# Optimization experiments

Hardware: AMD Instinct MI355X
Metric: run time of the kernel (lower is better)

The kernel has to match this reference:

```python
import jax, jax.numpy as jnp
import numpy as np

EMB_DIM = 1024
N_HEAD = 16
HEAD_DIM = EMB_DIM // N_HEAD  # 64
NUM_KV = 1
SEQ = 2048
BATCH = 2
QKV_OUT = (N_HEAD + 2 * NUM_KV) * HEAD_DIM  # 1152
ROPE_THETA = 10000.0


def _rope_tables(seq_len, dim):
    inv_freq = 1.0 / (ROPE_THETA ** (jnp.arange(0, dim, 2, dtype=jnp.float32) / dim))  # [dim/2]
    pos = jnp.arange(seq_len, dtype=jnp.float32)
    ang = pos[:, None] * inv_freq[None, :]  # [S, dim/2]
    return jnp.cos(ang), jnp.sin(ang)


def _apply_rope(x, cos, sin):
    # x: [B, S, H, D]; interleaved-pair rotation (torchtune-style)
    B, S, H, D = x.shape
    xr = x.reshape(B, S, H, D // 2, 2)
    x1, x2 = xr[..., 0], xr[..., 1]
    c = cos[None, :, None, :]
    s = sin[None, :, None, :]
    o1 = x1 * c - x2 * s
    o2 = x1 * s + x2 * c
    return jnp.stack([o1, o2], axis=-1).reshape(B, S, H, D)


def setup_inputs() -> dict:
    key = jax.random.key(0)
    k1, k2, k3, k4, k5 = jax.random.split(key, 5)
    scale = 1.0 / np.sqrt(EMB_DIM)
    return {
        "x": jax.random.normal(k1, (BATCH, SEQ, EMB_DIM), dtype=jnp.float32),
        "qkv_w": jax.random.uniform(k2, (QKV_OUT, EMB_DIM), jnp.float32, -scale, scale),
        "qkv_b": jax.random.uniform(k3, (QKV_OUT,), jnp.float32, -scale, scale),
        "out_w": jax.random.uniform(k4, (EMB_DIM, EMB_DIM), jnp.float32, -scale, scale),
        "out_b": jax.random.uniform(k5, (EMB_DIM,), jnp.float32, -scale, scale),
    }


def reference(x, qkv_w, qkv_b, out_w, out_b):
    B, S, E = x.shape
    qkv = x @ qkv_w.T + qkv_b  # [B, S, 1152]
    q_size = N_HEAD * HEAD_DIM
    kv_size = NUM_KV * HEAD_DIM
    q = qkv[..., :q_size].reshape(B, S, N_HEAD, HEAD_DIM)
    k = qkv[..., q_size:q_size + kv_size].reshape(B, S, NUM_KV, HEAD_DIM)
    v = qkv[..., q_size + kv_size:].reshape(B, S, NUM_KV, HEAD_DIM)

    cos, sin = _rope_tables(S, HEAD_DIM)
    q = _apply_rope(q, cos, sin)
    k = _apply_rope(k, cos, sin)

    q = q.transpose(0, 2, 1, 3)  # [B, H, S, D]
    k = k.transpose(0, 2, 1, 3)  # [B, 1, S, D]
    v = v.transpose(0, 2, 1, 3)  # [B, 1, S, D]

    # MQA: single KV head broadcasts over N_HEAD query heads
    scores = jnp.matmul(q, jnp.swapaxes(k, -2, -1)) / np.sqrt(HEAD_DIM)  # [B,H,S,S]
    causal = jnp.tril(jnp.ones((S, S), dtype=bool))
    scores = jnp.where(causal[None, None, :, :], scores, -jnp.inf)
    attn = jax.nn.softmax(scores, axis=-1)
    out = jnp.matmul(attn, v)  # [B, H, S, D]
    out = out.transpose(0, 2, 1, 3).reshape(B, S, E)
    return out @ out_w.T + out_b
```

## Files before the change

kernel.cpp:

```cpp
#include <hip/hip_runtime.h>
#include <stdint.h>
#include <stddef.h>

#define SEQ   2048
#define EMB   1024
#define NHEAD 16
#define HDIM  64
#define QKVO  1152
#define MTOT  4096

typedef __attribute__((ext_vector_type(4))) float f32x4;
typedef __attribute__((ext_vector_type(8))) short short8;
typedef __attribute__((ext_vector_type(4))) short s16x4;

__device__ __forceinline__ short f2bf(float f) {
  union { float f; unsigned u; } v; v.f = f;
  unsigned r = v.u + 0x7FFFu + ((v.u >> 16) & 1u);
  return (short)(r >> 16);
}

__device__ __forceinline__ void gload16(const void* g, void* l) {
  __builtin_amdgcn_global_load_lds((const __attribute__((address_space(1))) void*)g,
                                   (__attribute__((address_space(3))) void*)l,
                                   16, 0, 0);
}

#define PX   524288
#define PW1  671744
#define PW2  802816
#define PTOT 811008

__device__ __forceinline__ void cvt8(const float* __restrict__ s, short* __restrict__ d) {
  float4 a = ((const float4*)s)[0];
  float4 b = ((const float4*)s)[1];
  short8 r;
  r[0]=f2bf(a.x); r[1]=f2bf(a.y); r[2]=f2bf(a.z); r[3]=f2bf(a.w);
  r[4]=f2bf(b.x); r[5]=f2bf(b.y); r[6]=f2bf(b.z); r[7]=f2bf(b.w);
  *(short8*)d = r;
}

__global__ __launch_bounds__(256) void prep_kernel(
    const float* __restrict__ x, const float* __restrict__ wqkv, const float* __restrict__ wout,
    short* __restrict__ xb, short* __restrict__ wqkvb, short* __restrict__ woutb,
    float* __restrict__ cost, float* __restrict__ sint) {
  int c = blockIdx.x * 256 + threadIdx.x;
  if (c < PX) {
    cvt8(x + (size_t)c * 8, xb + (size_t)c * 8);
  } else if (c < PW1) {
    int c2 = c - PX;
    cvt8(wqkv + (size_t)c2 * 8, wqkvb + (size_t)c2 * 8);
  } else if (c < PW2) {
    int c2 = c - PW1;
    cvt8(wout + (size_t)c2 * 8, woutb + (size_t)c2 * 8);
  } else if (c < PTOT) {
    int c2 = c - PW2;
    #pragma unroll
    for (int t = 0; t < 8; ++t) {
      int idx = c2 * 8 + t;
      int pos = idx >> 5, i = idx & 31;
      float inv = powf(10000.0f, -(float)i * (1.0f / 32.0f));
      float ang = (float)pos * inv;
      float sv, cv;
      sincosf(ang, &sv, &cv);
      cost[idx] = cv; sint[idx] = sv;
    }
  }
}

__device__ __forceinline__ void gemm_mainloop(
    const short* __restrict__ A, const short* __restrict__ Bm,
    int m0, int n0, short* lsA, short* lsB, f32x4 acc[4][4]) {
  const int w = threadIdx.x >> 6, lane = threadIdx.x & 63;
  const int wm = w >> 1, wn = w & 1;
  const int lrow = lane & 15, lk = (lane >> 4) * 8;
  #pragma unroll
  for (int mi = 0; mi < 4; ++mi)
    #pragma unroll
    for (int ni = 0; ni < 4; ++ni)
      acc[mi][ni] = (f32x4){0.f, 0.f, 0.f, 0.f};

  const int srow8 = lane >> 3;
  const int scol = (lane & 7) * 8;

  for (int kt = 0; kt < 1024; kt += 64) {
    #pragma unroll
    for (int ii = 0; ii < 4; ++ii) {
      int seg = w * 4 + ii;
      int row = seg * 8 + srow8;
      gload16(A  + (size_t)(m0 + row) * 1024 + kt + scol, lsA + seg * 512);
      gload16(Bm + (size_t)(n0 + row) * 1024 + kt + scol, lsB + seg * 512);
    }
    __syncthreads();
    #pragma unroll
    for (int ks = 0; ks < 2; ++ks) {
      short8 af[4], bfv[4];
      #pragma unroll
      for (int mi = 0; mi < 4; ++mi)
        af[mi] = *(const short8*)(lsA + (wm * 64 + mi * 16 + lrow) * 64 + lk + ks * 32);
      #pragma unroll
      for (int ni = 0; ni < 4; ++ni)
        bfv[ni] = *(const short8*)(lsB + (wn * 64 + ni * 16 + lrow) * 64 + lk + ks * 32);
      #pragma unroll
      for (int mi = 0; mi < 4; ++mi)
        #pragma unroll
        for (int ni = 0; ni < 4; ++ni)
          acc[mi][ni] = __builtin_amdgcn_mfma_f32_16x16x32_bf16(af[mi], bfv[ni], acc[mi][ni], 0, 0, 0);
    }
    __syncthreads();
  }
}

#define QSCALE 0.180336880111124f

__global__ __launch_bounds__(256) void qkv_kernel(
    const short* __restrict__ xb, const short* __restrict__ wb,
    const float* __restrict__ bias, const float* __restrict__ cost, const float* __restrict__ sint,
    short* __restrict__ qbuf, short* __restrict__ kbuf, short* __restrict__ vt) {
  __shared__ __align__(16) short lsA[8192];
  __shared__ __align__(16) short lsB[8192];
  f32x4 acc[4][4];
  const int m0 = blockIdx.x * 128, n0 = blockIdx.y * 128;
  gemm_mainloop(xb, wb, m0, n0, lsA, lsB, acc);

  const int w = threadIdx.x >> 6, lane = threadIdx.x & 63;
  const int wm = w >> 1, wn = w & 1;
  const int colb = n0 + wn * 64 + (lane & 15);
  const int rowb = m0 + wm * 64 + ((lane >> 4) << 2);
  #pragma unroll
  for (int ni = 0; ni < 4; ++ni) {
    const int col = colb + ni * 16;
    const float bv = bias[col];
    #pragma unroll
    for (int mi = 0; mi < 4; ++mi) {
      #pragma unroll
      for (int j = 0; j < 4; ++j) {
        const int m = rowb + mi * 16 + j;
        const int bb = m >> 11, pos = m & 2047;
        float v = acc[mi][ni][j] + bv;
        float vp = __shfl_xor(v, 1);
        float ov;
        if (col < 1088) {
          const int d = (col < 1024) ? (col & 63) : (col - 1024);
          const int i = d >> 1;
          const float cv = cost[pos * 32 + i], sv = sint[pos * 32 + i];
          ov = ((col & 1) == 0) ? (v * cv - vp * sv)
                                : (vp * sv + v * cv);
          if (col < 1024) ov *= QSCALE;
        } else {
          ov = v;
        }
        const short bfo = f2bf(ov);
        if (col < 1024) {
          const int h = col >> 6;
          qbuf[(((size_t)bb * NHEAD + h) * SEQ + pos) * HDIM + (col & 63)] = bfo;
        } else if (col < 1088) {
          kbuf[((size_t)bb * SEQ + pos) * HDIM + (col - 1024)] = bfo;
        } else {
          vt[((size_t)bb * HDIM + (col - 1088)) * SEQ + pos] = bfo;
        }
      }
    }
  }
}

#define PSTRIDE 72

__device__ __forceinline__ void stage_kv(
    const short* __restrict__ kb_b, const short* __restrict__ vt_b, int kv0,
    short* Kb, short* Vb, int tid) {
  #pragma unroll
  for (int rd = 0; rd < 2; ++rd) {
    const int ci = rd * 256 + tid;
    const int r = ci >> 3;
    const int cs = ((ci & 7) * 8) ^ ((r & 7) << 3);
    gload16(kb_b + (size_t)(kv0 + r) * HDIM + cs, Kb + ci * 8);
  }
  #pragma unroll
  for (int rd = 0; rd < 2; ++rd) {
    const int ci = rd * 256 + tid;
    const int r = ci >> 3;
    const int cs = ((ci & 7) * 8) ^ ((r & 7) << 3);
    gload16(vt_b + (size_t)r * SEQ + kv0 + cs, Vb + ci * 8);
  }
}

template<bool MASKED>
__device__ __forceinline__ void attn_tile(
    const short* __restrict__ Kb, const short* __restrict__ Vb,
    int kv0, int qg, int g, int sadr0, int sadr1,
    short* pls,
    short8 qf0, short8 qf1, float& m_run, float& l_run, f32x4 o[4]) {
  f32x4 st[4];
  #pragma unroll
  for (int r = 0; r < 4; ++r) {
    short8 k0 = *(const short8*)(Kb + sadr0 + r * 1024);
    short8 k1 = *(const short8*)(Kb + sadr1 + r * 1024);
    f32x4 z = (f32x4){0.f, 0.f, 0.f, 0.f};
    z = __builtin_amdgcn_mfma_f32_16x16x32_bf16(k0, qf0, z, 0, 0, 0);
    z = __builtin_amdgcn_mfma_f32_16x16x32_bf16(k1, qf1, z, 0, 0, 0);
    st[r] = z;
  }
  float s[16];
  #pragma unroll
  for (int r = 0; r < 4; ++r)
    #pragma unroll
    for (int j = 0; j < 4; ++j) {
      if (MASKED) {
        const int kv = kv0 + r * 16 + g * 4 + j;
        s[r * 4 + j] = (kv <= qg) ? st[r][j] : -1.0e38f;
      } else {
        s[r * 4 + j] = st[r][j];
      }
    }
  float mt = s[0];
  #pragma unroll
  for (int i = 1; i < 16; ++i) mt = fmaxf(mt, s[i]);
  mt = fmaxf(mt, __shfl_xor(mt, 16));
  mt = fmaxf(mt, __shfl_xor(mt, 32));
  if (!__all(mt <= m_run + 11.0f)) {
    const float m_new = fmaxf(m_run, mt);
    const float sc = __builtin_amdgcn_exp2f(m_run - m_new);
    #pragma unroll
    for (int nf = 0; nf < 4; ++nf) o[nf] *= sc;
    l_run *= sc;
    m_run = m_new;
  }
  float p[16], ps = 0.f;
  #pragma unroll
  for (int i = 0; i < 16; ++i) { p[i] = __builtin_amdgcn_exp2f(s[i] - m_run); ps += p[i]; }
  ps += __shfl_xor(ps, 16);
  ps += __shfl_xor(ps, 32);
  l_run += ps;
  #pragma unroll
  for (int r = 0; r < 4; ++r)
    #pragma unroll
    for (int jj = 0; jj < 4; jj += 2) {
      unsigned pk = (unsigned)(unsigned short)f2bf(p[r * 4 + jj]) |
                    ((unsigned)(unsigned short)f2bf(p[r * 4 + jj + 1]) << 16);
      *(unsigned*)(pls + r * 16 + g * 4 + jj) = pk;
    }
  short8 pb0 = *(const short8*)(pls + g * 8);
  short8 pb1 = *(const short8*)(pls + 32 + g * 8);
  #pragma unroll
  for (int nf = 0; nf < 4; ++nf) {
    short8 v0 = *(const short8*)(Vb + sadr0 + nf * 1024);
    short8 v1 = *(const short8*)(Vb + sadr1 + nf * 1024);
    o[nf] = __builtin_amdgcn_mfma_f32_16x16x32_bf16(v0, pb0, o[nf], 0, 0, 0);
    o[nf] = __builtin_amdgcn_mfma_f32_16x16x32_bf16(v1, pb1, o[nf], 0, 0, 0);
  }
}

__global__ __launch_bounds__(256, 3) void attn_kernel(
    const short* __restrict__ qb, const short* __restrict__ kb,
    const short* __restrict__ vt, short* __restrict__ ao) {
  __shared__ __align__(16) short Kls[2][4096];
  __shared__ __align__(16) short Vls[2][4096];
  __shared__ __align__(16) short plds[4][16][PSTRIDE];
  const int tid = threadIdx.x, w = tid >> 6, lane = tid & 63;
  const int bh = blockIdx.x, bb = bh >> 4, h = bh & 15;
  const int qchunk = 31 - blockIdx.y;
  const int q0 = qchunk * 64 + w * 16;
  const int g = lane >> 4, qloc = lane & 15;
  const int qg = q0 + qloc;

  const short* kb_b = kb + (size_t)bb * SEQ * HDIM;
  const short* vt_b = vt + (size_t)bb * HDIM * SEQ;

  const short* qbase = qb + (((size_t)bb * NHEAD + h) * SEQ + q0 + qloc) * HDIM + g * 8;
  short8 qf0 = *(const short8*)qbase;
  short8 qf1 = *(const short8*)(qbase + 32);

  f32x4 o[4];
  #pragma unroll
  for (int nf = 0; nf < 4; ++nf) o[nf] = (f32x4){0.f, 0.f, 0.f, 0.f};
  float m_run = -1.0e38f, l_run = 0.0f;

  short* pls = &plds[w][qloc][0];
  const int swm = (qloc & 7) << 3;
  const int sadr0 = qloc * 64 + ((g * 8) ^ swm);
  const int sadr1 = qloc * 64 + ((g * 8 + 32) ^ swm);

  stage_kv(kb_b, vt_b, 0, Kls[0], Vls[0], tid);
  const int nt = qchunk + 1;
  for (int t = 0; t < nt; ++t) {
    if (t + 1 < nt) {
      stage_kv(kb_b, vt_b, (t + 1) * 64, Kls[(t + 1) & 1], Vls[(t + 1) & 1], tid);
      asm volatile("s_waitcnt vmcnt(4)" ::: "memory");
    } else {
      asm volatile("s_waitcnt vmcnt(0)" ::: "memory");
    }
    __builtin_amdgcn_sched_barrier(0);
    __builtin_amdgcn_s_barrier();
    __builtin_amdgcn_sched_barrier(0);
    const short* Kb = Kls[t & 1];
    const short* Vb = Vls[t & 1];
    if (t + 1 < nt)
      attn_tile<false>(Kb, Vb, t * 64, qg, g, sadr0, sadr1, pls, qf0, qf1, m_run, l_run, o);
    else
      attn_tile<true>(Kb, Vb, t * 64, qg, g, sadr0, sadr1, pls, qf0, qf1, m_run, l_run, o);
    __builtin_amdgcn_sched_barrier(0);
    __builtin_amdgcn_s_barrier();
  }

  const float inv = 1.0f / l_run;
  const size_t obase = ((size_t)bb * SEQ + q0 + qloc) * EMB + (size_t)h * HDIM + g * 4;
  #pragma unroll
  for (int nf = 0; nf < 4; ++nf) {
    s16x4 pk;
    #pragma unroll
    for (int j = 0; j < 4; ++j) pk[j] = f2bf(o[nf][j] * inv);
    *(s16x4*)(ao + obase + nf * 16) = pk;
  }
}

__global__ __launch_bounds__(256) void out_kernel(
    const short* __restrict__ ab, const short* __restrict__ wb,
    const float* __restrict__ bias, float* __restrict__ out) {
  __shared__ __align__(16) short lsA[8192];
  __shared__ __align__(16) short lsB[8192];
  f32x4 acc[4][4];
  const int m0 = blockIdx.x * 128, n0 = blockIdx.y * 128;
  gemm_mainloop(ab, wb, m0, n0, lsA, lsB, acc);

  const int w = threadIdx.x >> 6, lane = threadIdx.x & 63;
  const int wm = w >> 1, wn = w & 1;
  const int colb = n0 + wn * 64 + (lane & 15);
  const int rowb = m0 + wm * 64 + ((lane >> 4) << 2);
  #pragma unroll
  for (int ni = 0; ni < 4; ++ni) {
    const int col = colb + ni * 16;
    const float bv = bias[col];
    #pragma unroll
    for (int mi = 0; mi < 4; ++mi)
      #pragma unroll
      for (int j = 0; j < 4; ++j) {
        const int m = rowb + mi * 16 + j;
        out[(size_t)m * EMB + col] = acc[mi][ni][j] + bv;
      }
  }
}

extern "C" void kernel_launch(void* const* d_in, const int* in_sizes, int n_in,
                              void* d_out, int out_size, void* d_ws, size_t ws_size,
                              hipStream_t stream) {
  const float* x    = (const float*)d_in[0];
  const float* qkvw = (const float*)d_in[1];
  const float* qkvb = (const float*)d_in[2];
  const float* outw = (const float*)d_in[3];
  const float* outb = (const float*)d_in[4];
  float* out = (float*)d_out;
  char* ws = (char*)d_ws;

  short* xb    = (short*)(ws + 0);
  short* wqkvb = (short*)(ws + 8388608);
  short* woutb = (short*)(ws + 10747904);
  float* cost  = (float*)(ws + 12845056);
  float* sint  = (float*)(ws + 13107200);
  short* qbuf  = (short*)(ws + 13369344);
  short* kbuf  = (short*)(ws + 21757952);
  short* vtb   = (short*)(ws + 22282240);
  short* aob   = xb;

  prep_kernel<<<3168, 256, 0, stream>>>(x, qkvw, outw, xb, wqkvb, woutb, cost, sint);
  qkv_kernel<<<dim3(32, 9), 256, 0, stream>>>(xb, wqkvb, qkvb, cost, sint, qbuf, kbuf, vtb);
  attn_kernel<<<dim3(32, 32), 256, 0, stream>>>(qbuf, kbuf, vtb, aob);
  out_kernel<<<dim3(32, 8), 256, 0, stream>>>(aob, woutb, outb, out);
}
```

Before: 192.1 us.

## Double-buffer GEMM mainloop with swizzled LDS and tune attention scheduling

The shared GEMM mainloop now double-buffers its LDS tiles, prefetching the next K tile with global_load_lds while computing the current one, and applies an XOR swizzle to cut LDS bank conflicts. Its launch bounds are set to two blocks per CU because LDS use doubles. The attention kernel gains s_setprio around its MFMA sections, a tree max reduction, a packed bf16 conversion instruction, and a swizzled unpadded P buffer. It also raises occupancy to four blocks and reorders query chunks to balance causal work across the grid. The cost is higher LDS pressure in the GEMMs and relies on the v_cvt_pk_bf16_f32 instruction being available.

Measured after the change: 172.0 us. -10.5%, faster.

```diff
diff --git a/kernel.cpp b/kernel.cpp
--- a/kernel.cpp
+++ b/kernel.cpp
@@ -17,6 +17,12 @@
   union { float f; unsigned u; } v; v.f = f;
   unsigned r = v.u + 0x7FFFu + ((v.u >> 16) & 1u);
   return (short)(r >> 16);
+}
+
+__device__ __forceinline__ unsigned cvtpk_bf16(float lo, float hi) {
+  unsigned r;
+  asm("v_cvt_pk_bf16_f32 %0, %1, %2" : "=v"(r) : "v"(lo), "v"(hi));
+  return r;
 }
 
 __device__ __forceinline__ void gload16(const void* g, void* l) {
@@ -69,7 +75,7 @@
 
 __device__ __forceinline__ void gemm_mainloop(
     const short* __restrict__ A, const short* __restrict__ Bm,
-    int m0, int n0, short* lsA, short* lsB, f32x4 acc[4][4]) {
+    int m0, int n0, short* ls, f32x4 acc[4][4]) {
   const int w = threadIdx.x >> 6, lane = threadIdx.x & 63;
   const int wm = w >> 1, wn = w & 1;
   const int lrow = lane & 15, lk = (lane >> 4) * 8;
@@ -80,47 +86,62 @@
       acc[mi][ni] = (f32x4){0.f, 0.f, 0.f, 0.f};
 
   const int srow8 = lane >> 3;
-  const int scol = (lane & 7) * 8;
-
-  for (int kt = 0; kt < 1024; kt += 64) {
-    #pragma unroll
-    for (int ii = 0; ii < 4; ++ii) {
-      int seg = w * 4 + ii;
-      int row = seg * 8 + srow8;
-      gload16(A  + (size_t)(m0 + row) * 1024 + kt + scol, lsA + seg * 512);
-      gload16(Bm + (size_t)(n0 + row) * 1024 + kt + scol, lsB + seg * 512);
-    }
-    __syncthreads();
+  const int scol = ((lane & 7) * 8) ^ (srow8 << 3);
+  const int rswz = (lrow & 7) << 3;
+
+  #define GSTAGE(buf, kt)                                                     \
+    _Pragma("unroll")                                                         \
+    for (int ii = 0; ii < 4; ++ii) {                                          \
+      int seg = w * 4 + ii;                                                   \
+      int row = seg * 8 + srow8;                                              \
+      gload16(A  + (size_t)(m0 + row) * 1024 + (kt) + scol, (buf) + seg * 512);\
+      gload16(Bm + (size_t)(n0 + row) * 1024 + (kt) + scol, (buf) + 8192 + seg * 512);\
+    }
+
+  GSTAGE(ls, 0);
+  for (int t = 0; t < 16; ++t) {
+    short* cur = ls + (t & 1) * 16384;
+    short* nxt = ls + ((t + 1) & 1) * 16384;
+    if (t < 15) {
+      GSTAGE(nxt, (t + 1) * 64);
+      asm volatile("s_waitcnt vmcnt(8)" ::: "memory");
+    } else {
+      asm volatile("s_waitcnt vmcnt(0)" ::: "memory");
+    }
+    __builtin_amdgcn_sched_barrier(0);
+    __builtin_amdgcn_s_barrier();
+    __builtin_amdgcn_sched_barrier(0);
     #pragma unroll
     for (int ks = 0; ks < 2; ++ks) {
       short8 af[4], bfv[4];
       #pragma unroll
       for (int mi = 0; mi < 4; ++mi)
-        af[mi] = *(const short8*)(lsA + (wm * 64 + mi * 16 + lrow) * 64 + lk + ks * 32);
+        af[mi] = *(const short8*)(cur + (wm * 64 + mi * 16 + lrow) * 64 + ((lk + ks * 32) ^ rswz));
       #pragma unroll
       for (int ni = 0; ni < 4; ++ni)
-        bfv[ni] = *(const short8*)(lsB + (wn * 64 + ni * 16 + lrow) * 64 + lk + ks * 32);
+        bfv[ni] = *(const short8*)(cur + 8192 + (wn * 64 + ni * 16 + lrow) * 64 + ((lk + ks * 32) ^ rswz));
       #pragma unroll
       for (int mi = 0; mi < 4; ++mi)
         #pragma unroll
         for (int ni = 0; ni < 4; ++ni)
           acc[mi][ni] = __builtin_amdgcn_mfma_f32_16x16x32_bf16(af[mi], bfv[ni], acc[mi][ni], 0, 0, 0);
     }
-    __syncthreads();
-  }
+    __builtin_amdgcn_sched_barrier(0);
+    __builtin_amdgcn_s_barrier();
+  }
+  #undef GSTAGE
 }
 
 #define QSCALE 0.180336880111124f
 
-__global__ __launch_bounds__(256) void qkv_kernel(
+__global__ __launch_bounds__(256, 2) void qkv_kernel(
     const short* __restrict__ xb, const short* __restrict__ wb,
     const float* __restrict__ bias, const float* __restrict__ cost, const float* __restrict__ sint,
     short* __restrict__ qbuf, short* __restrict__ kbuf, short* __restrict__ vt) {
-  __shared__ __align__(16) short lsA[8192];
-  __shared__ __align__(16) short lsB[8192];
+  __shared__ __align__(16) short ls[32768];
   f32x4 acc[4][4];
   const int m0 = blockIdx.x * 128, n0 = blockIdx.y * 128;
-  gemm_mainloop(xb, wb, m0, n0, lsA, lsB, acc);
+  gemm_mainloop(xb, wb, m0, n0, ls, acc);
 
   const int w = threadIdx.x >> 6, lane = threadIdx.x & 63;
   const int wm = w >> 1, wn = w & 1;
@@ -163,34 +184,14 @@
   }
 }
 
-#define PSTRIDE 72
-
-__device__ __forceinline__ void stage_kv(
-    const short* __restrict__ kb_b, const short* __restrict__ vt_b, int kv0,
-    short* Kb, short* Vb, int tid) {
-  #pragma unroll
-  for (int rd = 0; rd < 2; ++rd) {
-    const int ci = rd * 256 + tid;
-    const int r = ci >> 3;
-    const int cs = ((ci & 7) * 8) ^ ((r & 7) << 3);
-    gload16(kb_b + (size_t)(kv0 + r) * HDIM + cs, Kb + ci * 8);
-  }
-  #pragma unroll
-  for (int rd = 0; rd < 2; ++rd) {
-    const int ci = rd * 256 + tid;
-    const int r = ci >> 3;
-    const int cs = ((ci & 7) * 8) ^ ((r & 7) << 3);
-    gload16(vt_b + (size_t)r * SEQ + kv0 + cs, Vb + ci * 8);
-  }
-}
-
 template<bool MASKED>
 __device__ __forceinline__ void attn_tile(
     const short* __restrict__ Kb, const short* __restrict__ Vb,
-    int kv0, int qg, int g, int sadr0, int sadr1,
+    int kv0, int qg, int g, int sadr0, int sadr1, int pswz,
     short* pls,
     short8 qf0, short8 qf1, float& m_run, float& l_run, f32x4 o[4]) {
   f32x4 st[4];
+  __builtin_amdgcn_s_setprio(1);
   #pragma unroll
   for (int r = 0; r < 4; ++r) {
     short8 k0 = *(const short8*)(Kb + sadr0 + r * 1024);
@@ -200,6 +201,7 @@
     z = __builtin_amdgcn_mfma_f32_16x16x32_bf16(k1, qf1, z, 0, 0, 0);
     st[r] = z;
   }
+  __builtin_amdgcn_s_setprio(0);
   float s[16];
   #pragma unroll
   for (int r = 0; r < 4; ++r)
@@ -212,9 +214,14 @@
         s[r * 4 + j] = st[r][j];
       }
     }
-  float mt = s[0];
-  #pragma unroll
-  for (int i = 1; i < 16; ++i) mt = fmaxf(mt, s[i]);
+  float a0 = fmaxf(fmaxf(s[0], s[1]), s[2]);
+  float a1 = fmaxf(fmaxf(s[3], s[4]), s[5]);
+  float a2 = fmaxf(fmaxf(s[6], s[7]), s[8]);
+  float a3 = fmaxf(fmaxf(s[9], s[10]), s[11]);
+  float a4 = fmaxf(fmaxf(s[12], s[13]), s[14]);
+  float b0 = fmaxf(fmaxf(a0, a1), a2);
+  float b1 = fmaxf(fmaxf(a3, a4), s[15]);
+  float mt = fmaxf(b0, b1);
   mt = fmaxf(mt, __shfl_xor(mt, 16));
   mt = fmaxf(mt, __shfl_xor(mt, 32));
   if (!__all(mt <= m_run + 11.0f)) {
@@ -235,12 +242,12 @@
   for (int r = 0; r < 4; ++r)
     #pragma unroll
     for (int jj = 0; jj < 4; jj += 2) {
-      unsigned pk = (unsigned)(unsigned short)f2bf(p[r * 4 + jj]) |
-                    ((unsigned)(unsigned short)f2bf(p[r * 4 + jj + 1]) << 16);
-      *(unsigned*)(pls + r * 16 + g * 4 + jj) = pk;
-    }
-  short8 pb0 = *(const short8*)(pls + g * 8);
-  short8 pb1 = *(const short8*)(pls + 32 + g * 8);
+      unsigned pk = cvtpk_bf16(p[r * 4 + jj], p[r * 4 + jj + 1]);
+      *(unsigned*)(pls + ((r * 16 + g * 4 + jj) ^ pswz)) = pk;
+    }
+  short8 pb0 = *(const short8*)(pls + ((g * 8) ^ pswz));
+  short8 pb1 = *(const short8*)(pls + ((32 + g * 8) ^ pswz));
+  __builtin_amdgcn_s_setprio(1);
   #pragma unroll
   for (int nf = 0; nf < 4; ++nf) {
     short8 v0 = *(const short8*)(Vb + sadr0 + nf * 1024);
@@ -248,17 +255,39 @@
     o[nf] = __builtin_amdgcn_mfma_f32_16x16x32_bf16(v0, pb0, o[nf], 0, 0, 0);
     o[nf] = __builtin_amdgcn_mfma_f32_16x16x32_bf16(v1, pb1, o[nf], 0, 0, 0);
   }
-}
-
-__global__ __launch_bounds__(256, 3) void attn_kernel(
+  __builtin_amdgcn_s_setprio(0);
+}
+
+__device__ __forceinline__ void stage_kv(
+    const short* __restrict__ kb_b, const short* __restrict__ vt_b, int kv0,
+    short* Kb, short* Vb, int tid) {
+  #pragma unroll
+  for (int rd = 0; rd < 2; ++rd) {
+    const int ci = rd * 256 + tid;
+    const int r = ci >> 3;
+    const int cs = ((ci & 7) * 8) ^ ((r & 7) << 3);
+    gload16(kb_b + (size_t)(kv0 + r) * HDIM + cs, Kb + ci * 8);
+  }
+  #pragma unroll
+  for (int rd = 0; rd < 2; ++rd) {
+    const int ci = rd * 256 + tid;
+    const int r = ci >> 3;
+    const int cs = ((ci & 7) * 8) ^ ((r & 7) << 3);
+    gload16(vt_b + (size_t)r * SEQ + kv0 + cs, Vb + ci * 8);
+  }
+}
+
+__global__ __launch_bounds__(256, 4) void attn_kernel(
     const short* __restrict__ qb, const short* __restrict__ kb,
     const short* __restrict__ vt, short* __restrict__ ao) {
   __shared__ __align__(16) short Kls[2][4096];
   __shared__ __align__(16) short Vls[2][4096];
-  __shared__ __align__(16) short plds[4][16][PSTRIDE];
+  __shared__ __align__(16) short plds[4][16][64];
   const int tid = threadIdx.x, w = tid >> 6, lane = tid & 63;
   const int bh = blockIdx.x, bb = bh >> 4, h = bh & 15;
-  const int qchunk = 31 - blockIdx.y;
+  const int yy = blockIdx.y, kk = yy >> 3, bq = yy & 7;
+  const int qchunk = (kk == 0) ? bq : (kk == 1) ? (15 - bq)
+                   : (kk == 2) ? (16 + bq) : (31 - bq);
   const int q0 = qchunk * 64 + w * 16;
   const int g = lane >> 4, qloc = lane & 15;
   const int qg = q0 + qloc;
@@ -276,6 +305,7 @@
   float m_run = -1.0e38f, l_run = 0.0f;
 
   short* pls = &plds[w][qloc][0];
+  const int pswz = (qloc & 7) << 3;
   const int swm = (qloc & 7) << 3;
   const int sadr0 = qloc * 64 + ((g * 8) ^ swm);
   const int sadr1 = qloc * 64 + ((g * 8 + 32) ^ swm);
@@ -295,9 +325,9 @@
     const short* Kb = Kls[t & 1];
     const short* Vb = Vls[t & 1];
     if (t + 1 < nt)
-      attn_tile<false>(Kb, Vb, t * 64, qg, g, sadr0, sadr1, pls, qf0, qf1, m_run, l_run, o);
+      attn_tile<false>(Kb, Vb, t * 64, qg, g, sadr0, sadr1, pswz, pls, qf0, qf1, m_run, l_run, o);
     else
-      attn_tile<true>(Kb, Vb, t * 64, qg, g, sadr0, sadr1, pls, qf0, qf1, m_run, l_run, o);
+      attn_tile<true>(Kb, Vb, t * 64, qg, g, sadr0, sadr1, pswz, pls, qf0, qf1, m_run, l_run, o);
     __builtin_amdgcn_sched_barrier(0);
     __builtin_amdgcn_s_barrier();
   }
@@ -313,14 +343,13 @@
   }
 }
 
-__global__ __launch_bounds__(256) void out_kernel(
+__global__ __launch_bounds__(256, 2) void out_kernel(
     const short* __restrict__ ab, const short* __restrict__ wb,
     const float* __restrict__ bias, float* __restrict__ out) {
-  __shared__ __align__(16) short lsA[8192];
-  __shared__ __align__(16) short lsB[8192];
+  __shared__ __align__(16) short ls[32768];
   f32x4 acc[4][4];
   const int m0 = blockIdx.x * 128, n0 = blockIdx.y * 128;
-  gemm_mainloop(ab, wb, m0, n0, lsA, lsB, acc);
+  gemm_mainloop(ab, wb, m0, n0, ls, acc);
 
   const int w = threadIdx.x >> 6, lane = threadIdx.x & 63;
   const int wm = w >> 1, wn = w & 1;
```
